# Optimization experiments

Hardware: AMD Instinct MI355X
Metric: run time of the kernel (lower is better)

## Reference

```python
import jax, jax.numpy as jnp
import numpy as np

HIDDEN = 2048
NUM_HEADS = 16
NUM_KV_HEADS = 8
HEAD_DIM = 128
EPS = 1e-6
ROPE_THETA = 10000.0
SEQ = 2048
Q_SIZE = NUM_HEADS * HEAD_DIM
KV_SIZE = NUM_KV_HEADS * HEAD_DIM


def rmsnorm_f32(x, w, eps=EPS):
    # RMSNormF32: normalize in float32, scale by weight
    xf = x.astype(jnp.float32)
    var = jnp.mean(xf * xf, axis=-1, keepdims=True)
    return xf * jax.lax.rsqrt(var + eps) * w.astype(jnp.float32)


def apply_rope(x, cos, sin):
    # x: [S, H, D]; cos/sin: [S, D//2] (neox-style half split)
    half = x.shape[-1] // 2
    x1, x2 = x[..., :half], x[..., half:]
    c = cos[:, None, :]
    s = sin[:, None, :]
    return jnp.concatenate([x1 * c - x2 * s, x2 * c + x1 * s], axis=-1)


def setup_inputs() -> dict:
    key = jax.random.key(0)
    ks = jax.random.split(key, 6)
    return {
        "positions": jnp.arange(SEQ, dtype=jnp.int32),
        "hidden_states": jax.random.normal(ks[0], (SEQ, HIDDEN), jnp.float32),
        "ln_weight": 1.0 + 0.1 * jax.random.normal(ks[1], (HIDDEN,), jnp.float32),
        "qkv_weight": 0.02 * jax.random.normal(ks[2], (Q_SIZE + 2 * KV_SIZE, HIDDEN), jnp.float32),
        "q_norm_weight": 1.0 + 0.1 * jax.random.normal(ks[3], (HEAD_DIM,), jnp.float32),
        "k_norm_weight": 1.0 + 0.1 * jax.random.normal(ks[4], (HEAD_DIM,), jnp.float32),
        "o_weight": 0.02 * jax.random.normal(ks[5], (HIDDEN, Q_SIZE), jnp.float32),
    }


def reference(positions, hidden_states, ln_weight, qkv_weight, q_norm_weight, k_norm_weight, o_weight):
    S = hidden_states.shape[0]
    # 1. input RMSNorm (f32)
    normalized = rmsnorm_f32(hidden_states, ln_weight)
    # 2. fused QKV projection (no bias)
    qkv = normalized @ qkv_weight.T  # [S, q_size + 2*kv_size]
    q = qkv[:, :Q_SIZE].reshape(S, NUM_HEADS, HEAD_DIM)
    k = qkv[:, Q_SIZE:Q_SIZE + KV_SIZE].reshape(S, NUM_KV_HEADS, HEAD_DIM)
    v = qkv[:, Q_SIZE + KV_SIZE:].reshape(S, NUM_KV_HEADS, HEAD_DIM)
    # 3. RoPE (neox half-split, cache built from theta)
    inv_freq = ROPE_THETA ** (-jnp.arange(0, HEAD_DIM, 2, dtype=jnp.float32) / HEAD_DIM)
    freqs = positions.astype(jnp.float32)[:, None] * inv_freq[None, :]  # [S, D/2]
    cos, sin = jnp.cos(freqs), jnp.sin(freqs)
    q = apply_rope(q, cos, sin)
    k = apply_rope(k, cos, sin)
    # 4. per-head q/k RMSNorm (applied after RoPE, as in source)
    q = rmsnorm_f32(q, q_norm_weight)
    k = rmsnorm_f32(k, k_norm_weight)
    # 5. GQA expand kv heads
    rep = NUM_HEADS // NUM_KV_HEADS
    k = jnp.repeat(k, rep, axis=1)  # [S, NH, D]
    v = jnp.repeat(v, rep, axis=1)
    # 6. naive causal attention
    scores = jnp.einsum('shd,thd->hst', q, k) / (HEAD_DIM ** 0.5)  # [NH, S, S]
    causal = jnp.triu(jnp.ones((S, S), dtype=bool), k=1)
    scores = jnp.where(causal[None, :, :], -jnp.inf, scores)
    attn = jax.nn.softmax(scores, axis=-1)
    attn = jnp.nan_to_num(attn, nan=0.0)
    out = jnp.einsum('hst,thd->shd', attn, v).reshape(S, Q_SIZE)
    # 7. output projection
    return out @ o_weight.T
```

## Files before the change

kernel.cpp:

```cpp
#include <hip/hip_runtime.h>
#include <hip/hip_bf16.h>
#include <stdint.h>

typedef unsigned short u16;
typedef __attribute__((ext_vector_type(4))) float f32x4;
typedef __attribute__((ext_vector_type(8))) __bf16 bf16x8;
typedef __attribute__((ext_vector_type(8))) unsigned short u16x8;
typedef __attribute__((ext_vector_type(4))) unsigned short u16x4;

#define SEQ 2048
#define HID 2048
#define HD  128

__device__ __forceinline__ float b2f(u16 v) {
    union { float f; unsigned u; } c; c.u = ((unsigned)v) << 16; return c.f;
}
__device__ __forceinline__ u16 f2b(float f) {
    union { float f; unsigned u; } c; c.f = f;
    unsigned r = c.u + 0x7fffu + ((c.u >> 16) & 1u);
    return (u16)(r >> 16);
}
__device__ __forceinline__ bf16x8 tob(u16x8 v) {
    union { u16x8 u; bf16x8 b; } c; c.u = v; return c.b;
}
__device__ __forceinline__ u16x8 ld8(const u16* p) { return *(const u16x8*)p; }

typedef const __attribute__((address_space(1))) unsigned int* gas_ptr;
typedef __attribute__((address_space(3))) unsigned int* las_ptr;
__device__ __forceinline__ void gld16(const void* g, void* l) {
    __builtin_amdgcn_global_load_lds((gas_ptr)g, (las_ptr)l, 16, 0, 0);
}

__global__ __launch_bounds__(256) void k_prep(const float* __restrict__ x,
                                              const float* __restrict__ w,
                                              u16* __restrict__ normed,
                                              const float* __restrict__ qkvw,
                                              u16* __restrict__ qkvwb) {
    const int b = blockIdx.x, t = threadIdx.x;
    if (b < 2048) {
        const int row = b;
        const float* xr = x + (size_t)row * HID + t * 8;
        f32x4 xa = *(const f32x4*)xr;
        f32x4 xb = *(const f32x4*)(xr + 4);
        float xf[8]; float ss = 0.f;
#pragma unroll
        for (int e = 0; e < 4; ++e) { xf[e] = xa[e]; xf[e + 4] = xb[e]; }
#pragma unroll
        for (int e = 0; e < 8; ++e) ss += xf[e] * xf[e];
#pragma unroll
        for (int m = 32; m; m >>= 1) ss += __shfl_xor(ss, m);
        __shared__ float red[4];
        if ((t & 63) == 0) red[t >> 6] = ss;
        __syncthreads();
        ss = red[0] + red[1] + red[2] + red[3];
        const float sc = rsqrtf(ss * (1.0f / HID) + 1e-6f);
        f32x4 wa = *(const f32x4*)(w + t * 8);
        f32x4 wb = *(const f32x4*)(w + t * 8 + 4);
        u16x8 ov;
#pragma unroll
        for (int e = 0; e < 4; ++e) {
            ov[e] = f2b(xf[e] * sc * wa[e]);
            ov[e + 4] = f2b(xf[e + 4] * sc * wb[e]);
        }
        *(u16x8*)(normed + (size_t)row * HID + t * 8) = ov;
    } else {
        const size_t i = ((size_t)(b - 2048) * 256 + t) * 8;
        f32x4 a = *(const f32x4*)(qkvw + i);
        f32x4 bb = *(const f32x4*)(qkvw + i + 4);
        u16x8 o;
#pragma unroll
        for (int e = 0; e < 4; ++e) { o[e] = f2b(a[e]); o[e + 4] = f2b(bb[e]); }
        *(u16x8*)(qkvwb + i) = o;
    }
}

__global__ __launch_bounds__(256) void k_conv(const float* __restrict__ src,
                                              u16* __restrict__ dst) {
    const size_t i = ((size_t)blockIdx.x * 256 + threadIdx.x) * 8;
    f32x4 a = *(const f32x4*)(src + i);
    f32x4 b = *(const f32x4*)(src + i + 4);
    u16x8 o;
#pragma unroll
    for (int e = 0; e < 4; ++e) { o[e] = f2b(a[e]); o[e + 4] = f2b(b[e]); }
    *(u16x8*)(dst + i) = o;
}

#define STAGE_H(buf, ht)                                                      \
    do {                                                                      \
        char* ap = (char*)&As[buf][0] + wave * 1024;                          \
        char* bp = (char*)&Bs[buf][0] + wave * 1024;                          \
        const u16* gA = ga + (size_t)(ht) * 32;                               \
        const u16* gB = gb + (size_t)(ht) * 32;                               \
        gld16(gA, ap);                                                        \
        gld16(gA + rowskip, ap + 4096);                                       \
        gld16(gB, bp);                                                        \
        gld16(gB + rowskip, bp + 4096);                                       \
    } while (0)

#define GEMM_PIPE(K)                                                          \
    STAGE_H(0, 0); STAGE_H(1, 1); STAGE_H(2, 2);                              \
    const int NH = (K) >> 5;                                                  \
    for (int ht = 0; ht < NH; ++ht) {                                         \
        if (ht <= NH - 3)      asm volatile("s_waitcnt vmcnt(8)" ::: "memory");\
        else if (ht == NH - 2) asm volatile("s_waitcnt vmcnt(4)" ::: "memory");\
        else                   asm volatile("s_waitcnt vmcnt(0)" ::: "memory");\
        __builtin_amdgcn_s_barrier();                                         \
        asm volatile("" ::: "memory");                                        \
        const u16* as = &As[ht & 3][0];                                       \
        const u16* bs = &Bs[ht & 3][0];                                       \
        bf16x8 af[4], bfr[4];                                                 \
        _Pragma("unroll")                                                     \
        for (int i = 0; i < 4; ++i)                                           \
            af[i] = tob(ld8(as + (wm * 64 + i * 16 + l16) * 32 + ((quad ^ sw) << 3))); \
        _Pragma("unroll")                                                     \
        for (int j = 0; j < 4; ++j)                                           \
            bfr[j] = tob(ld8(bs + (wn * 64 + j * 16 + l16) * 32 + ((quad ^ sw) << 3))); \
        __builtin_amdgcn_s_setprio(1);                                        \
        _Pragma("unroll")                                                     \
        for (int i = 0; i < 4; ++i)                                           \
            _Pragma("unroll")                                                 \
            for (int j = 0; j < 4; ++j)                                       \
                acc[i][j] = __builtin_amdgcn_mfma_f32_16x16x32_bf16(af[i], bfr[j], acc[i][j], 0, 0, 0); \
        __builtin_amdgcn_s_setprio(0);                                        \
        asm volatile("" ::: "memory");                                        \
        __builtin_amdgcn_s_barrier();                                         \
        if (ht + 3 < NH) { STAGE_H((ht + 3) & 3, ht + 3); }                   \
    }

__global__ __launch_bounds__(256) void k_gemm_qkv(const u16* __restrict__ A,
                                                  const u16* __restrict__ B,
                                                  u16* __restrict__ qraw,
                                                  u16* __restrict__ kraw,
                                                  u16* __restrict__ vtr,
                                                  int K) {
    __shared__ u16 As[4][128 * 32];
    __shared__ u16 Bs[4][128 * 32];
    const int tid = threadIdx.x;
    const int wave = tid >> 6, lane = tid & 63, quad = lane >> 4, l16 = lane & 15;
    const int wm = wave >> 1, wn = wave & 1;
    const int sw = (l16 >> 1) & 3;
    const int m0 = blockIdx.x * 128, n0 = blockIdx.y * 128;
    f32x4 acc[4][4];
#pragma unroll
    for (int i = 0; i < 4; ++i)
#pragma unroll
        for (int j = 0; j < 4; ++j) acc[i][j] = (f32x4){0.f, 0.f, 0.f, 0.f};

    const int gchunk = (tid & 3) ^ ((tid >> 3) & 3);
    const u16* ga = A + (size_t)(m0 + (tid >> 2)) * K + gchunk * 8;
    const u16* gb = B + (size_t)(n0 + (tid >> 2)) * K + gchunk * 8;
    const size_t rowskip = (size_t)64 * K;

    GEMM_PIPE(K)

#pragma unroll
    for (int i = 0; i < 4; ++i) {
        const int row = m0 + wm * 64 + i * 16 + quad * 4;
#pragma unroll
        for (int j = 0; j < 4; ++j) {
            const int col = n0 + wn * 64 + j * 16 + l16;
#pragma unroll
            for (int r = 0; r < 4; ++r) {
                const u16 val = f2b(acc[i][j][r]);
                const int s = row + r;
                if (col < 2048) {
                    const int head = col >> 7, d = col & 127;
                    qraw[((size_t)head * SEQ + s) * HD + d] = val;
                } else if (col < 3072) {
                    const int c = col - 2048, kv = c >> 7, d = c & 127;
                    kraw[((size_t)kv * SEQ + s) * HD + d] = val;
                } else {
                    const int c = col - 3072, kv = c >> 7, d = c & 127;
                    vtr[(size_t)kv * HD * SEQ + (size_t)d * SEQ + s] = val;
                }
            }
        }
    }
}

__global__ __launch_bounds__(256) void k_gemm_of(const u16* __restrict__ A,
                                                 const u16* __restrict__ B,
                                                 float* __restrict__ C,
                                                 int N, int K) {
    __shared__ u16 As[4][128 * 32];
    __shared__ u16 Bs[4][128 * 32];
    const int tid = threadIdx.x;
    const int wave = tid >> 6, lane = tid & 63, quad = lane >> 4, l16 = lane & 15;
    const int wm = wave >> 1, wn = wave & 1;
    const int sw = (l16 >> 1) & 3;
    const int m0 = blockIdx.x * 128, n0 = blockIdx.y * 128;
    f32x4 acc[4][4];
#pragma unroll
    for (int i = 0; i < 4; ++i)
#pragma unroll
        for (int j = 0; j < 4; ++j) acc[i][j] = (f32x4){0.f, 0.f, 0.f, 0.f};

    const int gchunk = (tid & 3) ^ ((tid >> 3) & 3);
    const u16* ga = A + (size_t)(m0 + (tid >> 2)) * K + gchunk * 8;
    const u16* gb = B + (size_t)(n0 + (tid >> 2)) * K + gchunk * 8;
    const size_t rowskip = (size_t)64 * K;

    GEMM_PIPE(K)

#pragma unroll
    for (int i = 0; i < 4; ++i) {
        const int row = m0 + wm * 64 + i * 16 + quad * 4;
#pragma unroll
        for (int j = 0; j < 4; ++j) {
            const int col = n0 + wn * 64 + j * 16 + l16;
#pragma unroll
            for (int r = 0; r < 4; ++r)
                C[(size_t)(row + r) * N + col] = acc[i][j][r];
        }
    }
}

__global__ __launch_bounds__(256) void k_ropenorm(const int* __restrict__ pos,
                                                  const float* __restrict__ qw,
                                                  const float* __restrict__ kw,
                                                  u16* __restrict__ qraw,
                                                  u16* __restrict__ kraw) {
    const int s = blockIdx.x;
    const int h = blockIdx.y * 4 + (threadIdx.x >> 6);
    const int d = threadIdx.x & 63;
    const bool isq = h < 16;
    u16* row = isq ? (qraw + ((size_t)h * SEQ + s) * HD)
                   : (kraw + ((size_t)(h - 16) * SEQ + s) * HD);
    const float x1 = b2f(row[d]), x2 = b2f(row[d + 64]);
    const float p = (float)pos[s];
    const float inv = exp2f(-(float)d * (2.0f / 128.0f) * 13.287712379549449f);
    const float fr = p * inv;
    const float c = cosf(fr), sn = sinf(fr);
    const float o1 = x1 * c - x2 * sn;
    const float o2 = x2 * c + x1 * sn;
    float ss = o1 * o1 + o2 * o2;
#pragma unroll
    for (int m = 32; m; m >>= 1) ss += __shfl_xor(ss, m);
    const float sc = rsqrtf(ss * (1.0f / HD) + 1e-6f);
    const float* w = isq ? qw : kw;
    row[d] = f2b(o1 * sc * w[d]);
    row[d + 64] = f2b(o2 * sc * w[d + 64]);
}

__global__ __launch_bounds__(256, 4) void k_attn(const u16* __restrict__ qh,
                                                 const u16* __restrict__ kh,
                                                 const u16* __restrict__ vt,
                                                 u16* __restrict__ out,
                                                 u16* __restrict__ po,
                                                 float* __restrict__ pl) {
    const int tid = threadIdx.x;
    const int wave = tid >> 6, lane = tid & 63, quad = lane >> 4, l16 = lane & 15;
    const int head = blockIdx.y;
    const int b = blockIdx.x;
    int qt, part, np;
    if (b < 11)      { qt = b;                      part = 0;            np = 1; }
    else if (b < 33) { qt = 11 + ((b - 11) >> 1);   part = (b - 11) & 1; np = 2; }
    else             { qt = 22 + (b - 33) / 3;      part = (b - 33) % 3; np = 3; }
    const int kvh = head >> 1;
    const int q0 = qt * 64;
    const int ntiles = qt + 1;

    __shared__ u16 Ks[64 * 128];
    __shared__ u16 Vts[128 * 64];
    __shared__ u16 Ps[4][16 * 64];

    const u16* qbase = qh + ((size_t)head * SEQ + q0 + wave * 16) * HD;
    bf16x8 aq[4];
#pragma unroll
    for (int kk = 0; kk < 4; ++kk)
        aq[kk] = tob(ld8(qbase + l16 * HD + kk * 32 + quad * 8));

    f32x4 acco[8];
#pragma unroll
    for (int j = 0; j < 8; ++j) acco[j] = (f32x4){0.f, 0.f, 0.f, 0.f};
    float lsum = 0.f;

    const float sc = 0.08838834764831845f;
    const u16* kbase = kh + (size_t)kvh * SEQ * HD;
    const u16* vbase = vt + (size_t)kvh * HD * SEQ;
    u16* pw = &Ps[wave][0];
    const int qrow_g = q0 + wave * 16 + l16;

    const u16* kg0 = kbase + (size_t)tid * 8;
    const u16* vg0 = vbase + (size_t)(tid >> 3) * SEQ + (size_t)(tid & 7) * 8;
    int kst[4], vst[4];
#pragma unroll
    for (int r = 0; r < 4; ++r) {
        const int krow = r * 16 + (tid >> 4);
        kst[r] = krow * 128 + (((tid & 15) ^ (krow & 7)) << 3);
        const int vrow = r * 32 + (tid >> 3);
        vst[r] = vrow * 64 + (((tid & 7) ^ (vrow & 7)) << 3);
    }

    u16x8 kreg[4], vreg[4];
    {
        const size_t koff = (size_t)part * 64;
#pragma unroll
        for (int r = 0; r < 4; ++r) {
            kreg[r] = ld8(kg0 + koff * HD + (size_t)r * 2048);
            vreg[r] = ld8(vg0 + koff + (size_t)r * 32 * SEQ);
        }
#pragma unroll
        for (int r = 0; r < 4; ++r) {
            *(u16x8*)(&Ks[0] + kst[r]) = kreg[r];
            *(u16x8*)(&Vts[0] + vst[r]) = vreg[r];
        }
    }
    __syncthreads();

    for (int kt = part; kt < ntiles; kt += np) {
        const bool havenext = (kt + np) < ntiles;
        if (havenext) {
            const size_t koff = (size_t)(kt + np) * 64;
#pragma unroll
            for (int r = 0; r < 4; ++r) {
                kreg[r] = ld8(kg0 + koff * HD + (size_t)r * 2048);
                vreg[r] = ld8(vg0 + koff + (size_t)r * 32 * SEQ);
            }
        }

        f32x4 accs[4];
#pragma unroll
        for (int j = 0; j < 4; ++j) accs[j] = (f32x4){0.f, 0.f, 0.f, 0.f};
#pragma unroll
        for (int kk = 0; kk < 4; ++kk) {
#pragma unroll
            for (int j = 0; j < 4; ++j) {
                const int krow = j * 16 + l16;
                const bf16x8 bk = tob(ld8(&Ks[0] + krow * 128 + (((kk * 4 + quad) ^ (krow & 7)) << 3)));
                accs[j] = __builtin_amdgcn_mfma_f32_16x16x32_bf16(bk, aq[kk], accs[j], 0, 0, 0);
            }
        }

        const int k0 = kt * 64;
#pragma unroll
        for (int j = 0; j < 4; ++j) {
            u16x4 pk;
#pragma unroll
            for (int r = 0; r < 4; ++r) {
                const int kpos = k0 + j * 16 + quad * 4 + r;
                const float pv = (kpos > qrow_g) ? 0.f : __expf(accs[j][r] * sc);
                lsum += pv;
                pk[r] = f2b(pv);
            }
            const int blk = (j * 2 + (quad >> 1)) ^ (l16 & 7);
            *(u16x4*)(pw + l16 * 64 + (blk << 3) + ((quad & 1) << 2)) = pk;
        }

#pragma unroll
        for (int kk = 0; kk < 2; ++kk) {
            const bf16x8 ap = tob(ld8(pw + l16 * 64 + (((kk * 4 + quad) ^ (l16 & 7)) << 3)));
#pragma unroll
            for (int j = 0; j < 8; ++j) {
                const int vrow = j * 16 + l16;
                const bf16x8 bv = tob(ld8(&Vts[0] + vrow * 64 + (((kk * 4 + quad) ^ (vrow & 7)) << 3)));
                acco[j] = __builtin_amdgcn_mfma_f32_16x16x32_bf16(ap, bv, acco[j], 0, 0, 0);
            }
        }

        __syncthreads();
        if (havenext) {
#pragma unroll
            for (int r = 0; r < 4; ++r) {
                *(u16x8*)(&Ks[0] + kst[r]) = kreg[r];
                *(u16x8*)(&Vts[0] + vst[r]) = vreg[r];
            }
        }
        __syncthreads();
    }

    float v = lsum;
    v += __shfl_xor(v, 16);
    v += __shfl_xor(v, 32);
    const int rowb = q0 + wave * 16 + quad * 4;

    if (np == 1) {
        f32x4 il;
#pragma unroll
        for (int r = 0; r < 4; ++r) il[r] = 1.0f / __shfl(v, quad * 4 + r);
#pragma unroll
        for (int j = 0; j < 8; ++j) {
            const int col = head * HD + j * 16 + l16;
#pragma unroll
            for (int r = 0; r < 4; ++r)
                out[(size_t)(rowb + r) * 2048 + col] = f2b(acco[j][r] * il[r]);
        }
    } else {
        u16* pob = po + (size_t)part * SEQ * 2048;
        float* plb = pl + (size_t)part * 16 * SEQ;
        if (lane < 16) plb[head * SEQ + q0 + wave * 16 + l16] = v;
#pragma unroll
        for (int j = 0; j < 8; ++j) {
            const int col = head * HD + j * 16 + l16;
#pragma unroll
            for (int r = 0; r < 4; ++r)
                pob[(size_t)(rowb + r) * 2048 + col] = f2b(acco[j][r]);
        }
    }
}

__global__ __launch_bounds__(256) void k_amerge(const u16* __restrict__ po,
                                                const float* __restrict__ pl,
                                                u16* __restrict__ out) {
    const int s = blockIdx.x + 704;
    const int qt = s >> 6;
    const int np = (qt > 21) ? 3 : 2;
    const int t = threadIdx.x;
    const int head = t >> 4;

    float l = 0.f;
#pragma unroll
    for (int p = 0; p < 3; ++p)
        if (p < np) l += pl[(size_t)p * 16 * SEQ + head * SEQ + s];
    const float il = 1.0f / l;

    float o[8] = {0.f, 0.f, 0.f, 0.f, 0.f, 0.f, 0.f, 0.f};
#pragma unroll
    for (int p = 0; p < 3; ++p) {
        if (p < np) {
            const u16x8 vv = ld8(po + (size_t)p * SEQ * 2048 + (size_t)s * 2048 + t * 8);
#pragma unroll
            for (int e = 0; e < 8; ++e) o[e] += b2f(vv[e]);
        }
    }
    u16x8 ov;
#pragma unroll
    for (int e = 0; e < 8; ++e) ov[e] = f2b(o[e] * il);
    *(u16x8*)(out + (size_t)s * 2048 + t * 8) = ov;
}

extern "C" void kernel_launch(void* const* d_in, const int* in_sizes, int n_in,
                              void* d_out, int out_size, void* d_ws, size_t ws_size,
                              hipStream_t stream) {
    const int*   positions = (const int*)d_in[0];
    const float* hidden   = (const float*)d_in[1];
    const float* lnw      = (const float*)d_in[2];
    const float* qkvw     = (const float*)d_in[3];
    const float* qnw      = (const float*)d_in[4];
    const float* knw      = (const float*)d_in[5];
    const float* ow       = (const float*)d_in[6];
    float* outp = (float*)d_out;

    char* ws = (char*)d_ws;
    const size_t MB = 1024ull * 1024ull;
    u16* normed = (u16*)(ws + 0 * MB);
    u16* qraw   = (u16*)(ws + 8 * MB);
    u16* kraw   = (u16*)(ws + 16 * MB);
    u16* vtr    = (u16*)(ws + 20 * MB);
    u16* qkvwb  = (u16*)(ws + 24 * MB);
    u16* owb    = (u16*)(ws + 0 * MB);
    u16* attno  = (u16*)(ws + 24 * MB);
    u16* po     = (u16*)(ws + 32 * MB);
    float* pl   = (float*)(ws + 56 * MB);

    k_prep    <<<6144, 256, 0, stream>>>(hidden, lnw, normed, qkvw, qkvwb);
    k_gemm_qkv<<<dim3(16, 32), 256, 0, stream>>>(normed, qkvwb, qraw, kraw, vtr, HID);
    k_ropenorm<<<dim3(SEQ, 6), 256, 0, stream>>>(positions, qnw, knw, qraw, kraw);
    k_conv    <<<2048, 256, 0, stream>>>(ow, owb);
    k_attn    <<<dim3(63, 16), 256, 0, stream>>>(qraw, kraw, vtr, attno, po, pl);
    k_amerge  <<<1344, 256, 0, stream>>>(po, pl, attno);
    k_gemm_of <<<dim3(16, 16), 256, 0, stream>>>(attno, owb, outp, HID, HID);
}
```

Measured before the change: 263.0 us.

## Load GEMM A fragments directly from global and double-buffer B in LDS

```diff
diff --git a/kernel.cpp b/kernel.cpp
--- a/kernel.cpp
+++ b/kernel.cpp
@@ -85,46 +85,51 @@
     *(u16x8*)(dst + i) = o;
 }
 
-#define STAGE_H(buf, ht)                                                      \
+#define STAGE_B(buf, k0)                                                      \
     do {                                                                      \
-        char* ap = (char*)&As[buf][0] + wave * 1024;                          \
-        char* bp = (char*)&Bs[buf][0] + wave * 1024;                          \
-        const u16* gA = ga + (size_t)(ht) * 32;                               \
-        const u16* gB = gb + (size_t)(ht) * 32;                               \
-        gld16(gA, ap);                                                        \
-        gld16(gA + rowskip, ap + 4096);                                       \
-        gld16(gB, bp);                                                        \
-        gld16(gB + rowskip, bp + 4096);                                       \
+        char* b0 = (char*)&Bs[buf][0][0] + wave * 1024;                       \
+        char* b1 = (char*)&Bs[buf][1][0] + wave * 1024;                       \
+        gld16(gb + (k0), b0);                                                 \
+        gld16(gb + (k0) + rowskip, b0 + 4096);                                \
+        gld16(gb + (k0) + 32, b1);                                            \
+        gld16(gb + (k0) + 32 + rowskip, b1 + 4096);                           \
     } while (0)
 
-#define GEMM_PIPE(K)                                                          \
-    STAGE_H(0, 0); STAGE_H(1, 1); STAGE_H(2, 2);                              \
-    const int NH = (K) >> 5;                                                  \
-    for (int ht = 0; ht < NH; ++ht) {                                         \
-        if (ht <= NH - 3)      asm volatile("s_waitcnt vmcnt(8)" ::: "memory");\
-        else if (ht == NH - 2) asm volatile("s_waitcnt vmcnt(4)" ::: "memory");\
-        else                   asm volatile("s_waitcnt vmcnt(0)" ::: "memory");\
+#define GEMM_LOOP(K)                                                          \
+    STAGE_B(0, 0);                                                            \
+    const int nk = (K) >> 6;                                                  \
+    for (int t = 0; t < nk; ++t) {                                            \
+        const int cur = t & 1;                                                \
+        const int k0 = t * 64;                                                \
+        asm volatile("s_waitcnt vmcnt(0)" ::: "memory");                      \
         __builtin_amdgcn_s_barrier();                                         \
         asm volatile("" ::: "memory");                                        \
-        const u16* as = &As[ht & 3][0];                                       \
-        const u16* bs = &Bs[ht & 3][0];                                       \
-        bf16x8 af[4], bfr[4];                                                 \
-        _Pragma("unroll")                                                     \
-        for (int i = 0; i < 4; ++i)                                           \
-            af[i] = tob(ld8(as + (wm * 64 + i * 16 + l16) * 32 + ((quad ^ sw) << 3))); \
+        bf16x8 a0[4], a1[4];                                                  \
+        _Pragma("unroll")                                                     \
+        for (int i = 0; i < 4; ++i) a0[i] = tob(ld8(arow[i] + k0));           \
+        _Pragma("unroll")                                                     \
+        for (int i = 0; i < 4; ++i) a1[i] = tob(ld8(arow[i] + k0 + 32));      \
+        if (t + 1 < nk) { STAGE_B(cur ^ 1, (t + 1) * 64); }                   \
+        bf16x8 bf0[4], bf1[4];                                                \
         _Pragma("unroll")                                                     \
         for (int j = 0; j < 4; ++j)                                           \
-            bfr[j] = tob(ld8(bs + (wn * 64 + j * 16 + l16) * 32 + ((quad ^ sw) << 3))); \
+            bf0[j] = tob(ld8(&Bs[cur][0][0] + (wn * 64 + j * 16 + l16) * 32 + ((quad ^ sw) << 3))); \
+        _Pragma("unroll")                                                     \
+        for (int j = 0; j < 4; ++j)                                           \
+            bf1[j] = tob(ld8(&Bs[cur][1][0] + (wn * 64 + j * 16 + l16) * 32 + ((quad ^ sw) << 3))); \
         __builtin_amdgcn_s_setprio(1);                                        \
         _Pragma("unroll")                                                     \
         for (int i = 0; i < 4; ++i)                                           \
             _Pragma("unroll")                                                 \
             for (int j = 0; j < 4; ++j)                                       \
-                acc[i][j] = __builtin_amdgcn_mfma_f32_16x16x32_bf16(af[i], bfr[j], acc[i][j], 0, 0, 0); \
+                acc[i][j] = __builtin_amdgcn_mfma_f32_16x16x32_bf16(a0[i], bf0[j], acc[i][j], 0, 0, 0); \
+        _Pragma("unroll")                                                     \
+        for (int i = 0; i < 4; ++i)                                           \
+            _Pragma("unroll")                                                 \
+            for (int j = 0; j < 4; ++j)                                       \
+                acc[i][j] = __builtin_amdgcn_mfma_f32_16x16x32_bf16(a1[i], bf1[j], acc[i][j], 0, 0, 0); \
         __builtin_amdgcn_s_setprio(0);                                        \
         asm volatile("" ::: "memory");                                        \
-        __builtin_amdgcn_s_barrier();                                         \
-        if (ht + 3 < NH) { STAGE_H((ht + 3) & 3, ht + 3); }                   \
     }
 
 __global__ __launch_bounds__(256) void k_gemm_qkv(const u16* __restrict__ A,
@@ -133,8 +138,7 @@
                                                   u16* __restrict__ kraw,
                                                   u16* __restrict__ vtr,
                                                   int K) {
-    __shared__ u16 As[4][128 * 32];
-    __shared__ u16 Bs[4][128 * 32];
+    __shared__ u16 Bs[2][2][128 * 32];
     const int tid = threadIdx.x;
     const int wave = tid >> 6, lane = tid & 63, quad = lane >> 4, l16 = lane & 15;
     const int wm = wave >> 1, wn = wave & 1;
@@ -147,11 +151,14 @@
         for (int j = 0; j < 4; ++j) acc[i][j] = (f32x4){0.f, 0.f, 0.f, 0.f};
 
     const int gchunk = (tid & 3) ^ ((tid >> 3) & 3);
-    const u16* ga = A + (size_t)(m0 + (tid >> 2)) * K + gchunk * 8;
     const u16* gb = B + (size_t)(n0 + (tid >> 2)) * K + gchunk * 8;
     const size_t rowskip = (size_t)64 * K;
-
-    GEMM_PIPE(K)
+    const u16* arow[4];
+#pragma unroll
+    for (int i = 0; i < 4; ++i)
+        arow[i] = A + (size_t)(m0 + wm * 64 + i * 16 + l16) * K + quad * 8;
+
+    GEMM_LOOP(K)
 
 #pragma unroll
     for (int i = 0; i < 4; ++i) {
@@ -182,8 +189,7 @@
                                                  const u16* __restrict__ B,
                                                  float* __restrict__ C,
                                                  int N, int K) {
-    __shared__ u16 As[4][128 * 32];
-    __shared__ u16 Bs[4][128 * 32];
+    __shared__ u16 Bs[2][2][128 * 32];
     const int tid = threadIdx.x;
     const int wave = tid >> 6, lane = tid & 63, quad = lane >> 4, l16 = lane & 15;
     const int wm = wave >> 1, wn = wave & 1;
@@ -196,11 +202,14 @@
         for (int j = 0; j < 4; ++j) acc[i][j] = (f32x4){0.f, 0.f, 0.f, 0.f};
 
     const int gchunk = (tid & 3) ^ ((tid >> 3) & 3);
-    const u16* ga = A + (size_t)(m0 + (tid >> 2)) * K + gchunk * 8;
     const u16* gb = B + (size_t)(n0 + (tid >> 2)) * K + gchunk * 8;
     const size_t rowskip = (size_t)64 * K;
-
-    GEMM_PIPE(K)
+    const u16* arow[4];
+#pragma unroll
+    for (int i = 0; i < 4; ++i)
+        arow[i] = A + (size_t)(m0 + wm * 64 + i * 16 + l16) * K + quad * 8;
+
+    GEMM_LOOP(K)
 
 #pragma unroll
     for (int i = 0; i < 4; ++i) {
```

After: 307.1 us. +16.8%, slower.
